# Optimization experiments

Hardware: AMD Instinct MI355X
Metric: run time of the kernel (lower is better)

The kernel has to match this reference:

```python
import jax, jax.numpy as jnp
from jax import lax
import numpy as np

B, T, F, H, L = 256, 512, 16, 256, 2


def _lstm_layer(x, w_ih, w_hh, b_ih, b_hh):
    # x: [B, T, in]; w_ih: [4H, in]; w_hh: [4H, H]; biases: [4H]
    # PyTorch gate order: i, f, g, o
    x_proj = jnp.einsum('bti,gi->btg', x, w_ih) + b_ih + b_hh  # [B, T, 4H]
    h0 = jnp.zeros((x.shape[0], w_hh.shape[1]), x.dtype)
    c0 = h0

    def step(carry, xp):
        h, c = carry
        gates = xp + h @ w_hh.T  # [B, 4H]
        i, f, g, o = jnp.split(gates, 4, axis=-1)
        c = jax.nn.sigmoid(f) * c + jax.nn.sigmoid(i) * jnp.tanh(g)
        h = jax.nn.sigmoid(o) * jnp.tanh(c)
        return (h, c), h

    _, hs = lax.scan(step, (h0, c0), jnp.swapaxes(x_proj, 0, 1))  # [T, B, H]
    return jnp.swapaxes(hs, 0, 1)  # [B, T, H]


def setup_inputs() -> dict:
    key = jax.random.key(0)
    ks = jax.random.split(key, 16)
    x = jax.random.normal(ks[0], (B, T, F), dtype=jnp.float32)
    lengths = jax.random.randint(ks[1], (B,), 1, T + 1)  # in [1, T]
    s = 1.0 / np.sqrt(H)
    u = lambda k, shape: jax.random.uniform(k, shape, jnp.float32, -s, s)
    inp = {'x': x, 'lengths': lengths}
    in_dims = [F, H]
    for l in range(L):
        inp[f'w_ih{l}'] = u(ks[2 + 4 * l], (4 * H, in_dims[l]))
        inp[f'w_hh{l}'] = u(ks[3 + 4 * l], (4 * H, H))
        inp[f'b_ih{l}'] = u(ks[4 + 4 * l], (4 * H,))
        inp[f'b_hh{l}'] = u(ks[5 + 4 * l], (4 * H,))
    inp['fc_w'] = u(ks[10], (1, H))
    inp['fc_b'] = u(ks[11], (1,))
    return inp


def reference(x, lengths, w_ih0, w_hh0, b_ih0, b_hh0,
              w_ih1, w_hh1, b_ih1, b_hh1, fc_w, fc_b):
    # Packed LSTM: outputs at t >= length never influence last_outputs
    # (recurrence only flows forward in time), so running the dense
    # full-length LSTM and gathering at lengths-1 is mathematically identical.
    h = _lstm_layer(x, w_ih0, w_hh0, b_ih0, b_hh0)
    h = _lstm_layer(h, w_ih1, w_hh1, b_ih1, b_hh1)
    last = h[jnp.arange(h.shape[0]), lengths - 1]  # [B, H]
    return jax.nn.relu(last) @ fc_w.T + fc_b  # [B, 1]
```

## Files before the change

### kernel.cpp

```cpp
#include <hip/hip_runtime.h>
#include <hip/hip_fp16.h>


#define Tc 32
#define NCHUNK 16

#define OFF_IH0   0
#define OFF_B0    16384
#define OFF_B1    17408
#define OFF_C0S   18432
#define OFF_C1S   84480
#define OFF_H1S   150528
#define OFF_HLAST 216576
#define FP_END    282624
#define H_HH0  0
#define H_HH1  262144
#define H_IH1  524288
#define H_H0C  786432
#define H0SLOT 2113536
#define H_XP1  5013504
#define XPSLOT 8454144

#define SMEM_BYTES 66560

typedef _Float16 v2h __attribute__((ext_vector_type(2)));

__device__ __forceinline__ unsigned packh2(float a, float b) {
  __half2 h = __floats2half2_rn(a, b);
  return *(unsigned*)&h;
}
__device__ __forceinline__ float4 dot4(const float4 w, const v2h h, float4 acc) {
  const v2h* wg = (const v2h*)&w;
  acc.x = __builtin_amdgcn_fdot2(wg[0], h, acc.x, false);
  acc.y = __builtin_amdgcn_fdot2(wg[1], h, acc.y, false);
  acc.z = __builtin_amdgcn_fdot2(wg[2], h, acc.z, false);
  acc.w = __builtin_amdgcn_fdot2(wg[3], h, acc.w, false);
  return acc;
}
__device__ __forceinline__ float sigf(float x) {
  return __fdividef(1.f, 1.f + __expf(-x));
}
__device__ __forceinline__ float tanhf_fast(float x) {
  float ax = fabsf(x);
  float e = __expf(-2.f * ax);
  float t = __fdividef(1.f - e, 1.f + e);
  return copysignf(t, x);
}
__device__ __forceinline__ float h2f(unsigned short s) {
  __half h = __builtin_bit_cast(__half, s);
  return __half2float(h);
}
__device__ __forceinline__ float4 cvt4(ushort4 v) {
  float4 r;
  r.x = h2f(v.x); r.y = h2f(v.y); r.z = h2f(v.z); r.w = h2f(v.w);
  return r;
}
__device__ __forceinline__ v2h u2h(unsigned v) {
  return __builtin_bit_cast(v2h, v);
}

__global__ __launch_bounds__(256) void prep_kernel(
    const float* __restrict__ w_ih0, const float* __restrict__ w_hh0,
    const float* __restrict__ b_ih0, const float* __restrict__ b_hh0,
    const float* __restrict__ w_ih1, const float* __restrict__ w_hh1,
    const float* __restrict__ b_ih1, const float* __restrict__ b_hh1,
    float* __restrict__ ws) {
  const int idx = blockIdx.x * blockDim.x + threadIdx.x;
  const int g = idx & 3, u = (idx >> 2) & 255, p = idx >> 10;
  const int j = g * 256 + u;
  unsigned* h16u = (unsigned*)(ws + FP_END);
  h16u[H_HH0 / 2 + idx] = packh2(w_hh0[j * 256 + 2 * p], w_hh0[j * 256 + 2 * p + 1]);
  h16u[H_HH1 / 2 + idx] = packh2(w_hh1[j * 256 + 2 * p], w_hh1[j * 256 + 2 * p + 1]);
  h16u[H_IH1 / 2 + idx] = packh2(w_ih1[j * 256 + 2 * p], w_ih1[j * 256 + 2 * p + 1]);
  if (idx < 8192) {
    ((unsigned*)(ws + OFF_IH0))[idx] =
        packh2(w_ih0[j * 16 + 2 * p], w_ih0[j * 16 + 2 * p + 1]);
  }
  if (idx < 1024) {
    ws[OFF_B0 + idx] = b_ih0[j] + b_hh0[j];
    ws[OFF_B1 + idx] = b_ih1[j] + b_hh1[j];
  }
}

__global__ __launch_bounds__(512, 2) void fused_kernel(
    float* __restrict__ ws, const float* __restrict__ x,
    const int* __restrict__ lengths, int step) {
  extern __shared__ __align__(16) char smem_raw[];
  const int bid = blockIdx.x;
  const int tid = threadIdx.x;
  __half* h16 = (__half*)(ws + FP_END);
  unsigned short* h0cS = (unsigned short*)(h16 + H_H0C);
  unsigned short* xpS = (unsigned short*)(h16 + H_XP1);

  if (bid < 86) {
    if (step >= NCHUNK) return;
    const int kc = step;
    const int kh = tid >> 8, u = tid & 255;
    const int bg = bid * 3;
    unsigned short* hb = (unsigned short*)smem_raw;
    unsigned* xsp = (unsigned*)(smem_raw + 4096);
    float* scratch = (float*)(smem_raw + 4352);
    float4* wxl = (float4*)(smem_raw + 18048);

    int len[3];
    #pragma unroll
    for (int b = 0; b < 3; ++b) len[b] = (bg + b < 256) ? lengths[bg + b] : 1;
    const int tmaxb = max(len[0], max(len[1], len[2]));
    if (kc * Tc >= tmaxb) return;
    const int tend = min(Tc, tmaxb - kc * Tc);
    const int slot = kc & 1, slotP = slot ^ 1;

    {
      const float4* gwx = (const float4*)(ws + OFF_IH0);
      #pragma unroll
      for (int e = 0; e < 4; ++e) wxl[tid + e * 512] = gwx[tid + e * 512];
    }

    const float4* wqR = (const float4*)(h16 + H_HH0) + (size_t)(kh * 64) * 256 + u;
    float4 wreg[32];
    #pragma unroll
    for (int p = 0; p < 32; ++p) wreg[p] = wqR[p * 256];
    const float4* wqS = wqR + 32 * 256;
    const float4 bias = ((const float4*)(ws + OFF_B0))[u];

    float c[3] = {0.f, 0.f, 0.f};
    if (kh == 0) {
      #pragma unroll
      for (int b = 0; b < 3; ++b) {
        unsigned short hv = 0;
        if (kc > 0) {
          hv = h0cS[(size_t)slotP * H0SLOT + ((size_t)(bg + b) * 32 + 31) * 256 + u];
          c[b] = ws[OFF_C0S + (bg + b) * 256 + u];
        }
        hb[0 * 768 + b * 256 + u] = hv;
      }
    }
    if (tid < 24) {
      int b = tid >> 3, i = tid & 7;
      int bb = min(bg + b, 255);
      const float* xp = x + (size_t)bb * 8192 + (kc * Tc) * 16;
      xsp[0 * 24 + b * 8 + i] = packh2(xp[2 * i], xp[2 * i + 1]);
    }
    __syncthreads();

    for (int tc = 0; tc < tend; ++tc) {
      const int cur = tc & 1, nxt = cur ^ 1;
      float4 A0, A1, A2;
      if (kh == 0) { A0 = bias; A1 = bias; A2 = bias; }
      else { A0 = make_float4(0, 0, 0, 0); A1 = A0; A2 = A0; }

      #pragma unroll
      for (int p = 0; p < 4; ++p) {
        float4 w = wxl[(kh * 4 + p) * 256 + u];
        v2h x0 = u2h(xsp[cur * 24 + 0 * 8 + kh * 4 + p]);
        v2h x1 = u2h(xsp[cur * 24 + 1 * 8 + kh * 4 + p]);
        v2h x2 = u2h(xsp[cur * 24 + 2 * 8 + kh * 4 + p]);
        A0 = dot4(w, x0, A0);
        A1 = dot4(w, x1, A1);
        A2 = dot4(w, x2, A2);
      }

      const float4* h0r0 = (const float4*)(hb + cur * 768 + 0 * 256 + kh * 128);
      const float4* h0r1 = (const float4*)(hb + cur * 768 + 1 * 256 + kh * 128);
      const float4* h0r2 = (const float4*)(hb + cur * 768 + 2 * 256 + kh * 128);

      #pragma unroll
      for (int grp = 0; grp < 8; ++grp) {
        float4 h40 = h0r0[grp], h41 = h0r1[grp], h42 = h0r2[grp];
        const v2h* hp0 = (const v2h*)&h40;
        const v2h* hp1 = (const v2h*)&h41;
        const v2h* hp2 = (const v2h*)&h42;
        #pragma unroll
        for (int q = 0; q < 4; ++q) {
          A0 = dot4(wreg[grp * 4 + q], hp0[q], A0);
          A1 = dot4(wreg[grp * 4 + q], hp1[q], A1);
          A2 = dot4(wreg[grp * 4 + q], hp2[q], A2);
        }
      }
      {
        float4 B[3][4];
        #pragma unroll
        for (int p = 0; p < 4; ++p) {
          B[0][p] = wqS[p * 256];
          B[1][p] = wqS[(4 + p) * 256];
        }
        #pragma unroll
        for (int g = 0; g < 8; ++g) {
          if (g + 2 < 8) {
            #pragma unroll
            for (int p = 0; p < 4; ++p)
              B[(g + 2) % 3][p] = wqS[((g + 2) * 4 + p) * 256];
          }
          const float4* wbuf = B[g % 3];
          float4 h40 = h0r0[8 + g], h41 = h0r1[8 + g], h42 = h0r2[8 + g];
          const v2h* hp0 = (const v2h*)&h40;
          const v2h* hp1 = (const v2h*)&h41;
          const v2h* hp2 = (const v2h*)&h42;
          #pragma unroll
          for (int q = 0; q < 4; ++q) {
            A0 = dot4(wbuf[q], hp0[q], A0);
            A1 = dot4(wbuf[q], hp1[q], A1);
            A2 = dot4(wbuf[q], hp2[q], A2);
          }
        }
      }

      if (kh == 1) {
        #pragma unroll
        for (int g = 0; g < 4; ++g) {
          scratch[u * 13 + g] = ((const float*)&A0)[g];
          scratch[u * 13 + 4 + g] = ((const float*)&A1)[g];
          scratch[u * 13 + 8 + g] = ((const float*)&A2)[g];
        }
        if (tid < 256 + 24) {
          int bi = tid - 256, b = bi >> 3, i = bi & 7;
          int bb = min(bg + b, 255);
          int tn = min(kc * Tc + tc + 1, 511);
          const float* xp = x + (size_t)bb * 8192 + tn * 16;
          xsp[nxt * 24 + b * 8 + i] = packh2(xp[2 * i], xp[2 * i + 1]);
        }
      }
      __syncthreads();
      if (kh == 0) {
        float4 B0, B1, B2;
        #pragma unroll
        for (int g = 0; g < 4; ++g) {
          ((float*)&B0)[g] = scratch[u * 13 + g];
          ((float*)&B1)[g] = scratch[u * 13 + 4 + g];
          ((float*)&B2)[g] = scratch[u * 13 + 8 + g];
        }
        A0.x += B0.x; A0.y += B0.y; A0.z += B0.z; A0.w += B0.w;
        A1.x += B1.x; A1.y += B1.y; A1.z += B1.z; A1.w += B1.w;
        A2.x += B2.x; A2.y += B2.y; A2.z += B2.z; A2.w += B2.w;
        float4 A[3] = {A0, A1, A2};
        #pragma unroll
        for (int b = 0; b < 3; ++b) {
          float ig = sigf(A[b].x), fg = sigf(A[b].y);
          float gg = tanhf_fast(A[b].z), og = sigf(A[b].w);
          c[b] = fg * c[b] + ig * gg;
          float h = og * tanhf_fast(c[b]);
          unsigned short hu = __half_as_ushort(__float2half(h));
          hb[nxt * 768 + b * 256 + u] = hu;
          h0cS[(size_t)slot * H0SLOT + ((size_t)(bg + b) * 32 + tc) * 256 + u] = hu;
        }
      }
      __syncthreads();
    }
    if (kh == 0) {
      #pragma unroll
      for (int b = 0; b < 3; ++b) ws[OFF_C0S + (bg + b) * 256 + u] = c[b];
    }

  } else if (bid < 172) {
    if (step < 2 || step >= NCHUNK + 2) return;
    const int kc = step - 2;
    const int kh = tid >> 8, u = tid & 255;
    const int bg = (bid - 86) * 3;
    unsigned short* h1b = (unsigned short*)smem_raw;
    float* scratch = (float*)(smem_raw + 4096);

    int len[3];
    #pragma unroll
    for (int b = 0; b < 3; ++b) len[b] = (bg + b < 256) ? lengths[bg + b] : 1;
    const int tmaxb = max(len[0], max(len[1], len[2]));
    if (kc * Tc >= tmaxb) return;
    const int tend = min(Tc, tmaxb - kc * Tc);
    const int slot = kc & 1;

    const float4* wqR = (const float4*)(h16 + H_HH1) + (size_t)(kh * 64) * 256 + u;
    float4 wreg[32];
    #pragma unroll
    for (int p = 0; p < 32; ++p) wreg[p] = wqR[p * 256];
    const float4* wqS = wqR + 32 * 256;

    float c[3] = {0.f, 0.f, 0.f}, hout[3] = {0.f, 0.f, 0.f};
    if (kh == 0) {
      #pragma unroll
      for (int b = 0; b < 3; ++b) {
        float hv = 0.f;
        if (kc > 0) {
          hv = ws[OFF_H1S + (bg + b) * 256 + u];
          c[b] = ws[OFF_C1S + (bg + b) * 256 + u];
        }
        h1b[0 * 768 + b * 256 + u] = __half_as_ushort(__float2half(hv));
      }
    }
    const unsigned short* xb =
        xpS + (size_t)slot * XPSLOT + (size_t)bg * 32768 + u * 4;
    ushort4 xc0, xc1, xc2;
    if (kh == 0) {
      xc0 = *(const ushort4*)(xb);
      xc1 = *(const ushort4*)(xb + 32768);
      xc2 = *(const ushort4*)(xb + 65536);
    }
    __syncthreads();

    for (int tc = 0; tc < tend; ++tc) {
      const int cur = tc & 1, nxt = cur ^ 1;
      float4 A0, A1, A2;
      ushort4 xn0, xn1, xn2;
      if (kh == 0) {
        A0 = cvt4(xc0); A1 = cvt4(xc1); A2 = cvt4(xc2);
        if (tc + 1 < tend) {
          xn0 = *(const ushort4*)(xb + (tc + 1) * 1024);
          xn1 = *(const ushort4*)(xb + 32768 + (tc + 1) * 1024);
          xn2 = *(const ushort4*)(xb + 65536 + (tc + 1) * 1024);
        }
      } else { A0 = make_float4(0, 0, 0, 0); A1 = A0; A2 = A0; }

      const float4* r0 = (const float4*)(h1b + cur * 768 + 0 * 256 + kh * 128);
      const float4* r1 = (const float4*)(h1b + cur * 768 + 1 * 256 + kh * 128);
      const float4* r2 = (const float4*)(h1b + cur * 768 + 2 * 256 + kh * 128);

      #pragma unroll
      for (int grp = 0; grp < 8; ++grp) {
        float4 h40 = r0[grp], h41 = r1[grp], h42 = r2[grp];
        const v2h* hp0 = (const v2h*)&h40;
        const v2h* hp1 = (const v2h*)&h41;
        const v2h* hp2 = (const v2h*)&h42;
        #pragma unroll
        for (int q = 0; q < 4; ++q) {
          A0 = dot4(wreg[grp * 4 + q], hp0[q], A0);
          A1 = dot4(wreg[grp * 4 + q], hp1[q], A1);
          A2 = dot4(wreg[grp * 4 + q], hp2[q], A2);
        }
      }
      {
        float4 B[3][4];
        #pragma unroll
        for (int p = 0; p < 4; ++p) {
          B[0][p] = wqS[p * 256];
          B[1][p] = wqS[(4 + p) * 256];
        }
        #pragma unroll
        for (int g = 0; g < 8; ++g) {
          if (g + 2 < 8) {
            #pragma unroll
            for (int p = 0; p < 4; ++p)
              B[(g + 2) % 3][p] = wqS[((g + 2) * 4 + p) * 256];
          }
          const float4* wbuf = B[g % 3];
          float4 h40 = r0[8 + g], h41 = r1[8 + g], h42 = r2[8 + g];
          const v2h* hp0 = (const v2h*)&h40;
          const v2h* hp1 = (const v2h*)&h41;
          const v2h* hp2 = (const v2h*)&h42;
          #pragma unroll
          for (int q = 0; q < 4; ++q) {
            A0 = dot4(wbuf[q], hp0[q], A0);
            A1 = dot4(wbuf[q], hp1[q], A1);
            A2 = dot4(wbuf[q], hp2[q], A2);
          }
        }
      }

      if (kh == 1) {
        #pragma unroll
        for (int g = 0; g < 4; ++g) {
          scratch[u * 13 + g] = ((const float*)&A0)[g];
          scratch[u * 13 + 4 + g] = ((const float*)&A1)[g];
          scratch[u * 13 + 8 + g] = ((const float*)&A2)[g];
        }
      }
      __syncthreads();
      if (kh == 0) {
        float4 B0, B1, B2;
        #pragma unroll
        for (int g = 0; g < 4; ++g) {
          ((float*)&B0)[g] = scratch[u * 13 + g];
          ((float*)&B1)[g] = scratch[u * 13 + 4 + g];
          ((float*)&B2)[g] = scratch[u * 13 + 8 + g];
        }
        A0.x += B0.x; A0.y += B0.y; A0.z += B0.z; A0.w += B0.w;
        A1.x += B1.x; A1.y += B1.y; A1.z += B1.z; A1.w += B1.w;
        A2.x += B2.x; A2.y += B2.y; A2.z += B2.z; A2.w += B2.w;
        float4 A[3] = {A0, A1, A2};
        const int t = kc * Tc + tc;
        #pragma unroll
        for (int b = 0; b < 3; ++b) {
          float ig = sigf(A[b].x), fg = sigf(A[b].y);
          float gg = tanhf_fast(A[b].z), og = sigf(A[b].w);
          c[b] = fg * c[b] + ig * gg;
          float h = og * tanhf_fast(c[b]);
          hout[b] = h;
          h1b[nxt * 768 + b * 256 + u] = __half_as_ushort(__float2half(h));
          if (t == len[b] - 1) ws[OFF_HLAST + (bg + b) * 256 + u] = h;
        }
        xc0 = xn0; xc1 = xn1; xc2 = xn2;
      }
      __syncthreads();
    }
    if (kh == 0) {
      #pragma unroll
      for (int b = 0; b < 3; ++b) {
        ws[OFF_C1S + (bg + b) * 256 + u] = c[b];
        ws[OFF_H1S + (bg + b) * 256 + u] = hout[b];
      }
    }

  } else {
    if (step < 1 || step >= NCHUNK + 1) return;
    if (bid >= 236) return;
    const int kc = step - 1;
    const int gid = bid - 172;
    const int b0g = gid * 4;
    const int rt = tid & 63, wv = tid >> 6;
    __half2* hc2 = (__half2*)smem_raw;

    int lmax = 0;
    #pragma unroll
    for (int i = 0; i < 4; ++i) lmax = max(lmax, lengths[b0g + i]);
    if (kc * Tc >= lmax) return;
    const int slot = kc & 1;

    {
      const unsigned short* src =
          h0cS + (size_t)slot * H0SLOT + (size_t)b0g * 8192;
      const int cl = tid & 127, pg = tid >> 7;
      #pragma unroll
      for (int pp = 0; pp < 32; pp += 4) {
        const int p0 = pg * 32 + pp;
        uint4 v = *(const uint4*)(src + (size_t)cl * 256 + p0 * 2);
        unsigned* d = (unsigned*)hc2;
        d[(p0 + 0) * 128 + cl] = v.x;
        d[(p0 + 1) * 128 + cl] = v.y;
        d[(p0 + 2) * 128 + cl] = v.z;
        d[(p0 + 3) * 128 + cl] = v.w;
      }
    }
    __syncthreads();

    const __half* Wb = h16 + H_IH1;
    unsigned short* xdst = xpS + (size_t)slot * XPSLOT;
    #pragma unroll 1
    for (int rp = 0; rp < 2; ++rp) {
      #pragma unroll 1
      for (int cp = 0; cp < 2; ++cp) {
        const int uA = rp * 128 + rt, uB = uA + 64;
        const int c0 = cp * 64 + wv * 8;
        const float4 bA = ((const float4*)(ws + OFF_B1))[uA];
        const float4 bB = ((const float4*)(ws + OFF_B1))[uB];
        float accA[4][8], accB[4][8];
        #pragma unroll
        for (int g = 0; g < 4; ++g)
          #pragma unroll
          for (int cc = 0; cc < 8; ++cc) {
            accA[g][cc] = ((const float*)&bA)[g];
            accB[g][cc] = ((const float*)&bB)[g];
          }
        #pragma unroll 2
        for (int p = 0; p < 128; ++p) {
          float4 wA = *(const float4*)(Wb + (size_t)p * 2048 + uA * 8);
          float4 wB = *(const float4*)(Wb + (size_t)p * 2048 + uB * 8);
          float4 h0v = *(const float4*)(hc2 + p * 128 + c0);
          float4 h1v = *(const float4*)(hc2 + p * 128 + c0 + 4);
          const v2h* ga = (const v2h*)&wA;
          const v2h* gb = (const v2h*)&wB;
          const v2h* hv = (const v2h*)&h0v;
          const v2h* hw = (const v2h*)&h1v;
          #pragma unroll
          for (int g = 0; g < 4; ++g) {
            #pragma unroll
            for (int cc = 0; cc < 4; ++cc) {
              accA[g][cc] = __builtin_amdgcn_fdot2(ga[g], hv[cc], accA[g][cc], false);
              accA[g][cc + 4] = __builtin_amdgcn_fdot2(ga[g], hw[cc], accA[g][cc + 4], false);
              accB[g][cc] = __builtin_amdgcn_fdot2(gb[g], hv[cc], accB[g][cc], false);
              accB[g][cc + 4] = __builtin_amdgcn_fdot2(gb[g], hw[cc], accB[g][cc + 4], false);
            }
          }
        }
        #pragma unroll
        for (int cc = 0; cc < 8; ++cc) {
          const int col = c0 + cc;
          const size_t cb = ((size_t)(b0g + (col >> 5)) * 32 + (col & 31)) * 1024;
          ushort4 oA, oB;
          oA.x = __half_as_ushort(__float2half(accA[0][cc]));
          oA.y = __half_as_ushort(__float2half(accA[1][cc]));
          oA.z = __half_as_ushort(__float2half(accA[2][cc]));
          oA.w = __half_as_ushort(__float2half(accA[3][cc]));
          oB.x = __half_as_ushort(__float2half(accB[0][cc]));
          oB.y = __half_as_ushort(__float2half(accB[1][cc]));
          oB.z = __half_as_ushort(__float2half(accB[2][cc]));
          oB.w = __half_as_ushort(__float2half(accB[3][cc]));
          *(ushort4*)(xdst + cb + uA * 4) = oA;
          *(ushort4*)(xdst + cb + uB * 4) = oB;
        }
      }
    }
  }
}

__global__ __launch_bounds__(256) void fc_kernel(
    const float* __restrict__ ws, const float* __restrict__ fc_w,
    const float* __restrict__ fc_b, float* __restrict__ out) {
  __shared__ float red[256];
  const int tid = threadIdx.x;
  const int b = blockIdx.x;
  red[tid] = fmaxf(ws[OFF_HLAST + b * 256 + tid], 0.f) * fc_w[tid];
  __syncthreads();
  #pragma unroll
  for (int s = 128; s > 0; s >>= 1) {
    if (tid < s) red[tid] += red[tid + s];
    __syncthreads();
  }
  if (tid == 0) out[b] = red[0] + fc_b[0];
}

extern "C" void kernel_launch(void* const* d_in, const int* in_sizes, int n_in,
                              void* d_out, int out_size, void* d_ws, size_t ws_size,
                              hipStream_t stream) {
  const float* x     = (const float*)d_in[0];
  const int*   lens  = (const int*)d_in[1];
  const float* w_ih0 = (const float*)d_in[2];
  const float* w_hh0 = (const float*)d_in[3];
  const float* b_ih0 = (const float*)d_in[4];
  const float* b_hh0 = (const float*)d_in[5];
  const float* w_ih1 = (const float*)d_in[6];
  const float* w_hh1 = (const float*)d_in[7];
  const float* b_ih1 = (const float*)d_in[8];
  const float* b_hh1 = (const float*)d_in[9];
  const float* fc_w  = (const float*)d_in[10];
  const float* fc_b  = (const float*)d_in[11];
  float* out = (float*)d_out;
  float* ws  = (float*)d_ws;

  hipLaunchKernelGGL(prep_kernel, dim3(512), dim3(256), 0, stream,
                     w_ih0, w_hh0, b_ih0, b_hh0, w_ih1, w_hh1, b_ih1, b_hh1, ws);
  hipFuncSetAttribute(reinterpret_cast<const void*>(fused_kernel),
                      hipFuncAttributeMaxDynamicSharedMemorySize, SMEM_BYTES);
  for (int k = 0; k < NCHUNK + 2; ++k) {
    hipLaunchKernelGGL(fused_kernel, dim3(236), dim3(512), SMEM_BYTES, stream,
                       ws, x, lens, k);
  }
  hipLaunchKernelGGL(fc_kernel, dim3(256), dim3(256), 0, stream,
                     ws, fc_w, fc_b, out);
}
```

Measured before the change: 3.145 ms.

## Split recurrent matvec four ways across 1024-thread blocks

Blocks grow from 512 to 1024 threads, and the hidden-dimension reduction of each recurrent step is split across four thread quarters instead of two. Partial sums are combined through shared memory, with each of three quarters then running the gate nonlinearity for one batch row, so that work is no longer serialised three rows per thread. The register-resident half of the weights is dropped and all recurrent weights are streamed from global memory each step. The layer-0 input projection moves to the fourth quarter, and the layer-1 input-projection GEMM spreads its row halves across the extra threads. This trades more weight reloads and a larger shared scratch for shorter per-step critical paths.

```diff
diff --git a/kernel.cpp b/kernel.cpp
--- a/kernel.cpp
+++ b/kernel.cpp
@@ -21,7 +21,7 @@
 #define H_XP1  5013504
 #define XPSLOT 8454144
 
-#define SMEM_BYTES 66560
+#define SMEM_BYTES 85184
 
 typedef _Float16 v2h __attribute__((ext_vector_type(2)));
 
@@ -57,6 +57,10 @@
 }
 __device__ __forceinline__ v2h u2h(unsigned v) {
   return __builtin_bit_cast(v2h, v);
+}
+__device__ __forceinline__ float4 f4add(float4 a, float4 b) {
+  a.x += b.x; a.y += b.y; a.z += b.z; a.w += b.w;
+  return a;
 }
 
 __global__ __launch_bounds__(256) void prep_kernel(
@@ -82,7 +86,7 @@
   }
 }
 
-__global__ __launch_bounds__(512, 2) void fused_kernel(
+__global__ __launch_bounds__(1024) void fused_kernel(
     float* __restrict__ ws, const float* __restrict__ x,
     const int* __restrict__ lengths, int step) {
   extern __shared__ __align__(16) char smem_raw[];
@@ -95,12 +99,12 @@
   if (bid < 86) {
     if (step >= NCHUNK) return;
     const int kc = step;
-    const int kh = tid >> 8, u = tid & 255;
+    const int kq = tid >> 8, u = tid & 255;
     const int bg = bid * 3;
     unsigned short* hb = (unsigned short*)smem_raw;
-    unsigned* xsp = (unsigned*)(smem_raw + 4096);
-    float* scratch = (float*)(smem_raw + 4352);
-    float4* wxl = (float4*)(smem_raw + 18048);
+    unsigned* xsp = (unsigned*)(smem_raw + 3072);
+    float4* sc4 = (float4*)(smem_raw + 3264);
+    float4* wxl = (float4*)(smem_raw + 52416);
 
     int len[3];
     #pragma unroll
@@ -112,28 +116,21 @@
 
     {
       const float4* gwx = (const float4*)(ws + OFF_IH0);
-      #pragma unroll
-      for (int e = 0; e < 4; ++e) wxl[tid + e * 512] = gwx[tid + e * 512];
-    }
-
-    const float4* wqR = (const float4*)(h16 + H_HH0) + (size_t)(kh * 64) * 256 + u;
-    float4 wreg[32];
-    #pragma unroll
-    for (int p = 0; p < 32; ++p) wreg[p] = wqR[p * 256];
-    const float4* wqS = wqR + 32 * 256;
+      wxl[tid] = gwx[tid];
+      wxl[tid + 1024] = gwx[tid + 1024];
+    }
+
+    const float4* wq = (const float4*)(h16 + H_HH0) + (size_t)(kq * 32) * 256 + u;
     const float4 bias = ((const float4*)(ws + OFF_B0))[u];
 
-    float c[3] = {0.f, 0.f, 0.f};
-    if (kh == 0) {
-      #pragma unroll
-      for (int b = 0; b < 3; ++b) {
-        unsigned short hv = 0;
-        if (kc > 0) {
-          hv = h0cS[(size_t)slotP * H0SLOT + ((size_t)(bg + b) * 32 + 31) * 256 + u];
-          c[b] = ws[OFF_C0S + (bg + b) * 256 + u];
-        }
-        hb[0 * 768 + b * 256 + u] = hv;
-      }
+    float cc = 0.f;
+    if (kq < 3) {
+      unsigned short hv = 0;
+      if (kc > 0) {
+        hv = h0cS[(size_t)slotP * H0SLOT + ((size_t)(bg + kq) * 32 + 31) * 256 + u];
+        cc = ws[OFF_C0S + (bg + kq) * 256 + u];
+      }
+      hb[0 * 768 + kq * 256 + u] = hv;
     }
     if (tid < 24) {
       int b = tid >> 3, i = tid & 7;
@@ -146,53 +143,38 @@
     for (int tc = 0; tc < tend; ++tc) {
       const int cur = tc & 1, nxt = cur ^ 1;
       float4 A0, A1, A2;
-      if (kh == 0) { A0 = bias; A1 = bias; A2 = bias; }
-      else { A0 = make_float4(0, 0, 0, 0); A1 = A0; A2 = A0; }
-
-      #pragma unroll
-      for (int p = 0; p < 4; ++p) {
-        float4 w = wxl[(kh * 4 + p) * 256 + u];
-        v2h x0 = u2h(xsp[cur * 24 + 0 * 8 + kh * 4 + p]);
-        v2h x1 = u2h(xsp[cur * 24 + 1 * 8 + kh * 4 + p]);
-        v2h x2 = u2h(xsp[cur * 24 + 2 * 8 + kh * 4 + p]);
-        A0 = dot4(w, x0, A0);
-        A1 = dot4(w, x1, A1);
-        A2 = dot4(w, x2, A2);
-      }
-
-      const float4* h0r0 = (const float4*)(hb + cur * 768 + 0 * 256 + kh * 128);
-      const float4* h0r1 = (const float4*)(hb + cur * 768 + 1 * 256 + kh * 128);
-      const float4* h0r2 = (const float4*)(hb + cur * 768 + 2 * 256 + kh * 128);
-
-      #pragma unroll
-      for (int grp = 0; grp < 8; ++grp) {
-        float4 h40 = h0r0[grp], h41 = h0r1[grp], h42 = h0r2[grp];
-        const v2h* hp0 = (const v2h*)&h40;
-        const v2h* hp1 = (const v2h*)&h41;
-        const v2h* hp2 = (const v2h*)&h42;
-        #pragma unroll
-        for (int q = 0; q < 4; ++q) {
-          A0 = dot4(wreg[grp * 4 + q], hp0[q], A0);
-          A1 = dot4(wreg[grp * 4 + q], hp1[q], A1);
-          A2 = dot4(wreg[grp * 4 + q], hp2[q], A2);
-        }
-      }
+      if (kq == 3) {
+        A0 = bias; A1 = bias; A2 = bias;
+        #pragma unroll
+        for (int p = 0; p < 8; ++p) {
+          float4 w = wxl[p * 256 + u];
+          A0 = dot4(w, u2h(xsp[cur * 24 + 0 * 8 + p]), A0);
+          A1 = dot4(w, u2h(xsp[cur * 24 + 1 * 8 + p]), A1);
+          A2 = dot4(w, u2h(xsp[cur * 24 + 2 * 8 + p]), A2);
+        }
+      } else {
+        A0 = make_float4(0, 0, 0, 0); A1 = A0; A2 = A0;
+      }
+
       {
+        const float4* h0r0 = (const float4*)(hb + cur * 768 + 0 * 256 + kq * 64);
+        const float4* h0r1 = (const float4*)(hb + cur * 768 + 1 * 256 + kq * 64);
+        const float4* h0r2 = (const float4*)(hb + cur * 768 + 2 * 256 + kq * 64);
         float4 B[3][4];
         #pragma unroll
         for (int p = 0; p < 4; ++p) {
-          B[0][p] = wqS[p * 256];
-          B[1][p] = wqS[(4 + p) * 256];
+          B[0][p] = wq[p * 256];
+          B[1][p] = wq[(4 + p) * 256];
         }
         #pragma unroll
         for (int g = 0; g < 8; ++g) {
           if (g + 2 < 8) {
             #pragma unroll
             for (int p = 0; p < 4; ++p)
-              B[(g + 2) % 3][p] = wqS[((g + 2) * 4 + p) * 256];
+              B[(g + 2) % 3][p] = wq[((g + 2) * 4 + p) * 256];
           }
           const float4* wbuf = B[g % 3];
-          float4 h40 = h0r0[8 + g], h41 = h0r1[8 + g], h42 = h0r2[8 + g];
+          float4 h40 = h0r0[g], h41 = h0r1[g], h42 = h0r2[g];
           const v2h* hp0 = (const v2h*)&h40;
           const v2h* hp1 = (const v2h*)&h41;
           const v2h* hp2 = (const v2h*)&h42;
@@ -205,59 +187,41 @@
         }
       }
 
-      if (kh == 1) {
-        #pragma unroll
-        for (int g = 0; g < 4; ++g) {
-          scratch[u * 13 + g] = ((const float*)&A0)[g];
-          scratch[u * 13 + 4 + g] = ((const float*)&A1)[g];
-          scratch[u * 13 + 8 + g] = ((const float*)&A2)[g];
-        }
-        if (tid < 256 + 24) {
-          int bi = tid - 256, b = bi >> 3, i = bi & 7;
-          int bb = min(bg + b, 255);
-          int tn = min(kc * Tc + tc + 1, 511);
-          const float* xp = x + (size_t)bb * 8192 + tn * 16;
-          xsp[nxt * 24 + b * 8 + i] = packh2(xp[2 * i], xp[2 * i + 1]);
-        }
-      }
+      sc4[(kq * 3 + 0) * 256 + u] = A0;
+      sc4[(kq * 3 + 1) * 256 + u] = A1;
+      sc4[(kq * 3 + 2) * 256 + u] = A2;
       __syncthreads();
-      if (kh == 0) {
-        float4 B0, B1, B2;
-        #pragma unroll
-        for (int g = 0; g < 4; ++g) {
-          ((float*)&B0)[g] = scratch[u * 13 + g];
-          ((float*)&B1)[g] = scratch[u * 13 + 4 + g];
-          ((float*)&B2)[g] = scratch[u * 13 + 8 + g];
-        }
-        A0.x += B0.x; A0.y += B0.y; A0.z += B0.z; A0.w += B0.w;
-        A1.x += B1.x; A1.y += B1.y; A1.z += B1.z; A1.w += B1.w;
-        A2.x += B2.x; A2.y += B2.y; A2.z += B2.z; A2.w += B2.w;
-        float4 A[3] = {A0, A1, A2};
-        #pragma unroll
-        for (int b = 0; b < 3; ++b) {
-          float ig = sigf(A[b].x), fg = sigf(A[b].y);
-          float gg = tanhf_fast(A[b].z), og = sigf(A[b].w);
-          c[b] = fg * c[b] + ig * gg;
-          float h = og * tanhf_fast(c[b]);
-          unsigned short hu = __half_as_ushort(__float2half(h));
-          hb[nxt * 768 + b * 256 + u] = hu;
-          h0cS[(size_t)slot * H0SLOT + ((size_t)(bg + b) * 32 + tc) * 256 + u] = hu;
-        }
+
+      if (kq < 3) {
+        float4 A = f4add(f4add(sc4[(0 * 3 + kq) * 256 + u],
+                               sc4[(1 * 3 + kq) * 256 + u]),
+                         f4add(sc4[(2 * 3 + kq) * 256 + u],
+                               sc4[(3 * 3 + kq) * 256 + u]));
+        float ig = sigf(A.x), fg = sigf(A.y);
+        float gg = tanhf_fast(A.z), og = sigf(A.w);
+        cc = fg * cc + ig * gg;
+        float h = og * tanhf_fast(cc);
+        unsigned short hu = __half_as_ushort(__float2half(h));
+        hb[nxt * 768 + kq * 256 + u] = hu;
+        h0cS[(size_t)slot * H0SLOT + ((size_t)(bg + kq) * 32 + tc) * 256 + u] = hu;
+      } else if (tid >= 768 && tid < 792) {
+        int bi = tid - 768, b = bi >> 3, i = bi & 7;
+        int bb = min(bg + b, 255);
+        int tn = min(kc * Tc + tc + 1, 511);
+        const float* xp = x + (size_t)bb * 8192 + tn * 16;
+        xsp[nxt * 24 + b * 8 + i] = packh2(xp[2 * i], xp[2 * i + 1]);
       }
       __syncthreads();
     }
-    if (kh == 0) {
-      #pragma unroll
-      for (int b = 0; b < 3; ++b) ws[OFF_C0S + (bg + b) * 256 + u] = c[b];
-    }
+    if (kq < 3) ws[OFF_C0S + (bg + kq) * 256 + u] = cc;
 
   } else if (bid < 172) {
     if (step < 2 || step >= NCHUNK + 2) return;
     const int kc = step - 2;
-    const int kh = tid >> 8, u = tid & 255;
+    const int kq = tid >> 8, u = tid & 255;
     const int bg = (bid - 86) * 3;
     unsigned short* h1b = (unsigned short*)smem_raw;
-    float* scratch = (float*)(smem_raw + 4096);
+    float4* sc4 = (float4*)(smem_raw + 3072);
 
     int len[3];
     #pragma unroll
@@ -267,80 +231,48 @@
     const int tend = min(Tc, tmaxb - kc * Tc);
     const int slot = kc & 1;
 
-    const float4* wqR = (const float4*)(h16 + H_HH1) + (size_t)(kh * 64) * 256 + u;
-    float4 wreg[32];
-    #pragma unroll
-    for (int p = 0; p < 32; ++p) wreg[p] = wqR[p * 256];
-    const float4* wqS = wqR + 32 * 256;
-
-    float c[3] = {0.f, 0.f, 0.f}, hout[3] = {0.f, 0.f, 0.f};
-    if (kh == 0) {
-      #pragma unroll
-      for (int b = 0; b < 3; ++b) {
-        float hv = 0.f;
-        if (kc > 0) {
-          hv = ws[OFF_H1S + (bg + b) * 256 + u];
-          c[b] = ws[OFF_C1S + (bg + b) * 256 + u];
-        }
-        h1b[0 * 768 + b * 256 + u] = __half_as_ushort(__float2half(hv));
-      }
-    }
-    const unsigned short* xb =
-        xpS + (size_t)slot * XPSLOT + (size_t)bg * 32768 + u * 4;
-    ushort4 xc0, xc1, xc2;
-    if (kh == 0) {
-      xc0 = *(const ushort4*)(xb);
-      xc1 = *(const ushort4*)(xb + 32768);
-      xc2 = *(const ushort4*)(xb + 65536);
+    const float4* wq = (const float4*)(h16 + H_HH1) + (size_t)(kq * 32) * 256 + u;
+
+    float cc = 0.f, hout = 0.f;
+    int lenb = 1;
+    const unsigned short* xb = xpS;
+    ushort4 xc;
+    if (kq < 3) {
+      lenb = len[kq];
+      float hv = 0.f;
+      if (kc > 0) {
+        hv = ws[OFF_H1S + (bg + kq) * 256 + u];
+        cc = ws[OFF_C1S + (bg + kq) * 256 + u];
+      }
+      h1b[0 * 768 + kq * 256 + u] = __half_as_ushort(__float2half(hv));
+      xb = xpS + (size_t)slot * XPSLOT + (size_t)(bg + kq) * 32768 + u * 4;
+      xc = *(const ushort4*)(xb);
     }
     __syncthreads();
 
     for (int tc = 0; tc < tend; ++tc) {
       const int cur = tc & 1, nxt = cur ^ 1;
-      float4 A0, A1, A2;
-      ushort4 xn0, xn1, xn2;
-      if (kh == 0) {
-        A0 = cvt4(xc0); A1 = cvt4(xc1); A2 = cvt4(xc2);
-        if (tc + 1 < tend) {
-          xn0 = *(const ushort4*)(xb + (tc + 1) * 1024);
-          xn1 = *(const ushort4*)(xb + 32768 + (tc + 1) * 1024);
-          xn2 = *(const ushort4*)(xb + 65536 + (tc + 1) * 1024);
-        }
-      } else { A0 = make_float4(0, 0, 0, 0); A1 = A0; A2 = A0; }
-
-      const float4* r0 = (const float4*)(h1b + cur * 768 + 0 * 256 + kh * 128);
-      const float4* r1 = (const float4*)(h1b + cur * 768 + 1 * 256 + kh * 128);
-      const float4* r2 = (const float4*)(h1b + cur * 768 + 2 * 256 + kh * 128);
-
-      #pragma unroll
-      for (int grp = 0; grp < 8; ++grp) {
-        float4 h40 = r0[grp], h41 = r1[grp], h42 = r2[grp];
-        const v2h* hp0 = (const v2h*)&h40;
-        const v2h* hp1 = (const v2h*)&h41;
-        const v2h* hp2 = (const v2h*)&h42;
-        #pragma unroll
-        for (int q = 0; q < 4; ++q) {
-          A0 = dot4(wreg[grp * 4 + q], hp0[q], A0);
-          A1 = dot4(wreg[grp * 4 + q], hp1[q], A1);
-          A2 = dot4(wreg[grp * 4 + q], hp2[q], A2);
-        }
-      }
+      float4 A0 = make_float4(0, 0, 0, 0), A1 = A0, A2 = A0;
+
       {
+        const float4* r0 = (const float4*)(h1b + cur * 768 + 0 * 256 + kq * 64);
+        const float4* r1 = (const float4*)(h1b + cur * 768 + 1 * 256 + kq * 64);
+        const float4* r2 = (const float4*)(h1b + cur * 768 + 2 * 256 + kq * 64);
         float4 B[3][4];
         #pragma unroll
         for (int p = 0; p < 4; ++p) {
-          B[0][p] = wqS[p * 256];
-          B[1][p] = wqS[(4 + p) * 256];
+          B[0][p] = wq[p * 256];
+          B[1][p] = wq[(4 + p) * 256];
         }
         #pragma unroll
         for (int g = 0; g < 8; ++g) {
           if (g + 2 < 8) {
             #pragma unroll
             for (int p = 0; p < 4; ++p)
-              B[(g + 2) % 3][p] = wqS[((g + 2) * 4 + p) * 256];
+              B[(g + 2) % 3][p] = wq[((g + 2) * 4 + p) * 256];
           }
           const float4* wbuf = B[g % 3];
-          float4 h40 = r0[8 + g], h41 = r1[8 + g], h42 = r2[8 + g];
+          float4 h40 = r0[g], h41 = r1[g], h42 = r2[g];
           const v2h* hp0 = (const v2h*)&h40;
           const v2h* hp1 = (const v2h*)&h41;
           const v2h* hp2 = (const v2h*)&h42;
@@ -353,48 +285,34 @@
         }
       }
 
-      if (kh == 1) {
-        #pragma unroll
-        for (int g = 0; g < 4; ++g) {
-          scratch[u * 13 + g] = ((const float*)&A0)[g];
-          scratch[u * 13 + 4 + g] = ((const float*)&A1)[g];
-          scratch[u * 13 + 8 + g] = ((const float*)&A2)[g];
-        }
-      }
+      sc4[(kq * 3 + 0) * 256 + u] = A0;
+      sc4[(kq * 3 + 1) * 256 + u] = A1;
+      sc4[(kq * 3 + 2) * 256 + u] = A2;
       __syncthreads();
-      if (kh == 0) {
-        float4 B0, B1, B2;
-        #pragma unroll
-        for (int g = 0; g < 4; ++g) {
-          ((float*)&B0)[g] = scratch[u * 13 + g];
-          ((float*)&B1)[g] = scratch[u * 13 + 4 + g];
-          ((float*)&B2)[g] = scratch[u * 13 + 8 + g];
-        }
-        A0.x += B0.x; A0.y += B0.y; A0.z += B0.z; A0.w += B0.w;
-        A1.x += B1.x; A1.y += B1.y; A1.z += B1.z; A1.w += B1.w;
-        A2.x += B2.x; A2.y += B2.y; A2.z += B2.z; A2.w += B2.w;
-        float4 A[3] = {A0, A1, A2};
+
+      if (kq < 3) {
+        ushort4 xn;
+        if (tc + 1 < tend) xn = *(const ushort4*)(xb + (tc + 1) * 1024);
+        float4 A = f4add(f4add(sc4[(0 * 3 + kq) * 256 + u],
+                               sc4[(1 * 3 + kq) * 256 + u]),
+                         f4add(sc4[(2 * 3 + kq) * 256 + u],
+                               sc4[(3 * 3 + kq) * 256 + u]));
+        A = f4add(A, cvt4(xc));
+        float ig = sigf(A.x), fg = sigf(A.y);
+        float gg = tanhf_fast(A.z), og = sigf(A.w);
+        cc = fg * cc + ig * gg;
+        float h = og * tanhf_fast(cc);
+        hout = h;
+        h1b[nxt * 768 + kq * 256 + u] = __half_as_ushort(__float2half(h));
         const int t = kc * Tc + tc;
-        #pragma unroll
-        for (int b = 0; b < 3; ++b) {
-          float ig = sigf(A[b].x), fg = sigf(A[b].y);
-          float gg = tanhf_fast(A[b].z), og = sigf(A[b].w);
-          c[b] = fg * c[b] + ig * gg;
-          float h = og * tanhf_fast(c[b]);
-          hout[b] = h;
-          h1b[nxt * 768 + b * 256 + u] = __half_as_ushort(__float2half(h));
-          if (t == len[b] - 1) ws[OFF_HLAST + (bg + b) * 256 + u] = h;
-        }
-        xc0 = xn0; xc1 = xn1; xc2 = xn2;
+        if (t == lenb - 1) ws[OFF_HLAST + (bg + kq) * 256 + u] = h;
+        xc = xn;
       }
       __syncthreads();
     }
-    if (kh == 0) {
-      #pragma unroll
-      for (int b = 0; b < 3; ++b) {
-        ws[OFF_C1S + (bg + b) * 256 + u] = c[b];
-        ws[OFF_H1S + (bg + b) * 256 + u] = hout[b];
-      }
+    if (kq < 3) {
+      ws[OFF_C1S + (bg + kq) * 256 + u] = cc;
+      ws[OFF_H1S + (bg + kq) * 256 + u] = hout;
     }
 
   } else {
@@ -403,7 +321,8 @@
     const int kc = step - 1;
     const int gid = bid - 172;
     const int b0g = gid * 4;
-    const int rt = tid & 63, wv = tid >> 6;
+    const int rp = tid >> 9;
+    const int rt = tid & 63, wv = (tid >> 6) & 7;
     __half2* hc2 = (__half2*)smem_raw;
 
     int lmax = 0;
@@ -417,8 +336,8 @@
           h0cS + (size_t)slot * H0SLOT + (size_t)b0g * 8192;
       const int cl = tid & 127, pg = tid >> 7;
       #pragma unroll
-      for (int pp = 0; pp < 32; pp += 4) {
-        const int p0 = pg * 32 + pp;
+      for (int pp = 0; pp < 16; pp += 4) {
+        const int p0 = pg * 16 + pp;
         uint4 v = *(const uint4*)(src + (size_t)cl * 256 + p0 * 2);
         unsigned* d = (unsigned*)hc2;
         d[(p0 + 0) * 128 + cl] = v.x;
@@ -432,58 +351,55 @@
     const __half* Wb = h16 + H_IH1;
     unsigned short* xdst = xpS + (size_t)slot * XPSLOT;
     #pragma unroll 1
-    for (int rp = 0; rp < 2; ++rp) {
-      #pragma unroll 1
-      for (int cp = 0; cp < 2; ++cp) {
-        const int uA = rp * 128 + rt, uB = uA + 64;
-        const int c0 = cp * 64 + wv * 8;
-        const float4 bA = ((const float4*)(ws + OFF_B1))[uA];
-        const float4 bB = ((const float4*)(ws + OFF_B1))[uB];
-        float accA[4][8], accB[4][8];
-        #pragma unroll
-        for (int g = 0; g < 4; ++g)
+    for (int cp = 0; cp < 2; ++cp) {
+      const int uA = rp * 128 + rt, uB = uA + 64;
+      const int c0 = cp * 64 + wv * 8;
+      const float4 bA = ((const float4*)(ws + OFF_B1))[uA];
+      const float4 bB = ((const float4*)(ws + OFF_B1))[uB];
+      float accA[4][8], accB[4][8];
+      #pragma unroll
+      for (int g = 0; g < 4; ++g)
+        #pragma unroll
+        for (int cc = 0; cc < 8; ++cc) {
+          accA[g][cc] = ((const float*)&bA)[g];
+          accB[g][cc] = ((const float*)&bB)[g];
+        }
+      #pragma unroll 2
+      for (int p = 0; p < 128; ++p) {
+        float4 wA = *(const float4*)(Wb + (size_t)p * 2048 + uA * 8);
+        float4 wB = *(const float4*)(Wb + (size_t)p * 2048 + uB * 8);
+        float4 h0v = *(const float4*)(hc2 + p * 128 + c0);
+        float4 h1v = *(const float4*)(hc2 + p * 128 + c0 + 4);
+        const v2h* ga = (const v2h*)&wA;
+        const v2h* gb = (const v2h*)&wB;
+        const v2h* hv = (const v2h*)&h0v;
+        const v2h* hw = (const v2h*)&h1v;
+        #pragma unroll
+        for (int g = 0; g < 4; ++g) {
           #pragma unroll
-          for (int cc = 0; cc < 8; ++cc) {
-            accA[g][cc] = ((const float*)&bA)[g];
-            accB[g][cc] = ((const float*)&bB)[g];
+          for (int cc = 0; cc < 4; ++cc) {
+            accA[g][cc] = __builtin_amdgcn_fdot2(ga[g], hv[cc], accA[g][cc], false);
+            accA[g][cc + 4] = __builtin_amdgcn_fdot2(ga[g], hw[cc], accA[g][cc + 4], false);
+            accB[g][cc] = __builtin_amdgcn_fdot2(gb[g], hv[cc], accB[g][cc], false);
+            accB[g][cc + 4] = __builtin_amdgcn_fdot2(gb[g], hw[cc], accB[g][cc + 4], false);
           }
-        #pragma unroll 2
-        for (int p = 0; p < 128; ++p) {
-          float4 wA = *(const float4*)(Wb + (size_t)p * 2048 + uA * 8);
-          float4 wB = *(const float4*)(Wb + (size_t)p * 2048 + uB * 8);
-          float4 h0v = *(const float4*)(hc2 + p * 128 + c0);
-          float4 h1v = *(const float4*)(hc2 + p * 128 + c0 + 4);
-          const v2h* ga = (const v2h*)&wA;
-          const v2h* gb = (const v2h*)&wB;
-          const v2h* hv = (const v2h*)&h0v;
-          const v2h* hw = (const v2h*)&h1v;
-          #pragma unroll
-          for (int g = 0; g < 4; ++g) {
-            #pragma unroll
-            for (int cc = 0; cc < 4; ++cc) {
-              accA[g][cc] = __builtin_amdgcn_fdot2(ga[g], hv[cc], accA[g][cc], false);
-              accA[g][cc + 4] = __builtin_amdgcn_fdot2(ga[g], hw[cc], accA[g][cc + 4], false);
-              accB[g][cc] = __builtin_amdgcn_fdot2(gb[g], hv[cc], accB[g][cc], false);
-              accB[g][cc + 4] = __builtin_amdgcn_fdot2(gb[g], hw[cc], accB[g][cc + 4], false);
-            }
-          }
-        }
-        #pragma unroll
-        for (int cc = 0; cc < 8; ++cc) {
-          const int col = c0 + cc;
-          const size_t cb = ((size_t)(b0g + (col >> 5)) * 32 + (col & 31)) * 1024;
-          ushort4 oA, oB;
-          oA.x = __half_as_ushort(__float2half(accA[0][cc]));
-          oA.y = __half_as_ushort(__float2half(accA[1][cc]));
-          oA.z = __half_as_ushort(__float2half(accA[2][cc]));
-          oA.w = __half_as_ushort(__float2half(accA[3][cc]));
-          oB.x = __half_as_ushort(__float2half(accB[0][cc]));
-          oB.y = __half_as_ushort(__float2half(accB[1][cc]));
-          oB.z = __half_as_ushort(__float2half(accB[2][cc]));
-          oB.w = __half_as_ushort(__float2half(accB[3][cc]));
-          *(ushort4*)(xdst + cb + uA * 4) = oA;
-          *(ushort4*)(xdst + cb + uB * 4) = oB;
-        }
+        }
+      }
+      #pragma unroll
+      for (int cc = 0; cc < 8; ++cc) {
+        const int col = c0 + cc;
+        const size_t cb = ((size_t)(b0g + (col >> 5)) * 32 + (col & 31)) * 1024;
+        ushort4 oA, oB;
+        oA.x = __half_as_ushort(__float2half(accA[0][cc]));
+        oA.y = __half_as_ushort(__float2half(accA[1][cc]));
+        oA.z = __half_as_ushort(__float2half(accA[2][cc]));
+        oA.w = __half_as_ushort(__float2half(accA[3][cc]));
+        oB.x = __half_as_ushort(__float2half(accB[0][cc]));
+        oB.y = __half_as_ushort(__float2half(accB[1][cc]));
+        oB.z = __half_as_ushort(__float2half(accB[2][cc]));
+        oB.w = __half_as_ushort(__float2half(accB[3][cc]));
+        *(ushort4*)(xdst + cb + uA * 4) = oA;
+        *(ushort4*)(xdst + cb + uB * 4) = oB;
       }
     }
   }
@@ -528,7 +444,7 @@
   hipFuncSetAttribute(reinterpret_cast<const void*>(fused_kernel),
                       hipFuncAttributeMaxDynamicSharedMemorySize, SMEM_BYTES);
   for (int k = 0; k < NCHUNK + 2; ++k) {
-    hipLaunchKernelGGL(fused_kernel, dim3(236), dim3(512), SMEM_BYTES, stream,
+    hipLaunchKernelGGL(fused_kernel, dim3(236), dim3(1024), SMEM_BYTES, stream,
                        ws, x, lens, k);
   }
   hipLaunchKernelGGL(fc_kernel, dim3(256), dim3(256), 0, stream,
```

Result: slower. 3.338 ms (+6.1%).
